# Optimization experiments

Hardware: AMD Instinct MI355X
Metric: run time of the kernel (lower is better)

The kernel has to match this reference:

```python
import jax, jax.numpy as jnp
import numpy as np

DIM = 384
HEADS = 12
HEAD_DIM = DIM // HEADS
SCALE = HEAD_DIM ** -0.5
HIDDEN = 4 * DIM
EPS = 1e-5


def _dwconv(x, w, b):
    # depthwise 3x3 conv, NCHW, kernel [C,1,3,3], groups=C
    y = jax.lax.conv_general_dilated(
        x, w, window_strides=(1, 1), padding='SAME',
        dimension_numbers=('NCHW', 'OIHW', 'NCHW'),
        feature_group_count=x.shape[1])
    return y + b[None, :, None, None]


def _layernorm(x, g, b):
    mu = jnp.mean(x, axis=-1, keepdims=True)
    var = jnp.mean(jnp.square(x - mu), axis=-1, keepdims=True)
    return (x - mu) * jax.lax.rsqrt(var + EPS) * g + b


def setup_inputs() -> dict:
    key = jax.random.key(0)
    ks = jax.random.split(key, 10)
    s = 0.02
    inp = {
        'x': jax.random.normal(ks[0], (32, DIM, 28, 28), dtype=jnp.float32),
        'cpe1_w': jax.random.normal(ks[1], (DIM, 1, 3, 3), dtype=jnp.float32) * s,
        'cpe1_b': jnp.zeros((DIM,), jnp.float32),
        'norm1_g': jnp.ones((DIM,), jnp.float32),
        'norm1_b': jnp.zeros((DIM,), jnp.float32),
        'qkv_w': jax.random.normal(ks[2], (3 * DIM, DIM), dtype=jnp.float32) * s,
        'proj_w': jax.random.normal(ks[3], (DIM, DIM), dtype=jnp.float32) * s,
        'proj_b': jnp.zeros((DIM,), jnp.float32),
        'cpe2_w': jax.random.normal(ks[4], (DIM, 1, 3, 3), dtype=jnp.float32) * s,
        'cpe2_b': jnp.zeros((DIM,), jnp.float32),
        'norm2_g': jnp.ones((DIM,), jnp.float32),
        'norm2_b': jnp.zeros((DIM,), jnp.float32),
        'fc1_w': jax.random.normal(ks[5], (HIDDEN, DIM), dtype=jnp.float32) * s,
        'fc1_b': jnp.zeros((HIDDEN,), jnp.float32),
        'fc2_w': jax.random.normal(ks[6], (DIM, HIDDEN), dtype=jnp.float32) * s,
        'fc2_b': jnp.zeros((DIM,), jnp.float32),
    }
    return inp


def reference(x, cpe1_w, cpe1_b, norm1_g, norm1_b, qkv_w, proj_w, proj_b,
              cpe2_w, cpe2_b, norm2_g, norm2_b, fc1_w, fc1_b, fc2_w, fc2_b):
    B, C, H, W = x.shape
    N = H * W
    # cpe1: depthwise conv residual (act = Identity)
    x = x + _dwconv(x, cpe1_w, cpe1_b)
    x = jnp.transpose(x.reshape(B, C, N), (0, 2, 1))  # [B, N, C]

    # channel attention
    cur = _layernorm(x, norm1_g, norm1_b)
    qkv = cur @ qkv_w.T  # [B, N, 3C]
    qkv = qkv.reshape(B, N, 3, HEADS, HEAD_DIM)
    q = qkv[:, :, 0]  # [B, N, h, d]
    k = qkv[:, :, 1] * SCALE
    v = qkv[:, :, 2]
    # attn = k^T @ v over tokens: [B, h, d, d]
    attn = jnp.einsum('bnhd,bnhe->bhde', k, v)
    attn = jax.nn.softmax(attn, axis=-1)
    # out[n,d] = sum_e attn[d,e] * q[n,e]
    out = jnp.einsum('bhde,bnhe->bnhd', attn, q).reshape(B, N, C)
    cur = out @ proj_w.T + proj_b
    x = x + cur

    # cpe2
    x = jnp.transpose(x, (0, 2, 1)).reshape(B, C, H, W)
    x = x + _dwconv(x, cpe2_w, cpe2_b)

    # MLP
    x = jnp.transpose(x.reshape(B, C, N), (0, 2, 1))  # [B, N, C]
    y = _layernorm(x, norm2_g, norm2_b)
    y = jax.nn.gelu(y @ fc1_w.T + fc1_b, approximate=False)
    y = y @ fc2_w.T + fc2_b
    x = x + y
    return jnp.transpose(x, (0, 2, 1)).reshape(B, C, H, W)
```

## Files before the change

kernel.cpp:

```cpp
#include <hip/hip_runtime.h>
#include <hip/hip_bf16.h>

#define CDIM 384
#define NHEADS 12
#define HDIM 32
#define HIDDEN 1536
#define BBATCH 32
#define HH 28
#define WW 28
#define NTOK 784
#define BN (BBATCH * NTOK)
#define LN_EPS 1e-5f
#define ATT_SCALE 0.17677669529663687f
#define YTILES 196
#define PERXCD 25

typedef __hip_bfloat16 bf16;
typedef __attribute__((ext_vector_type(8))) short bf16x8;
typedef __attribute__((ext_vector_type(4))) float f32x4;

__device__ __forceinline__ void stf(float* p, float v) { *p = v; }
__device__ __forceinline__ void stf(bf16* p, float v) { *p = __float2bfloat16(v); }

__device__ __forceinline__ short f2bs(float v) {
    bf16 t = __float2bfloat16(v);
    return *reinterpret_cast<short*>(&t);
}

__device__ __forceinline__ float bf2f(unsigned short u) {
    return __uint_as_float(((unsigned)u) << 16);
}

__device__ __forceinline__ float gelu_f(float x) {
    float u = x * (0.7978845608f + 0.0356774081f * x * x);
    float e = __expf(-2.f * u);
    return x / (1.f + e);
}

__device__ __forceinline__ void gload16(const void* g, void* l) {
    __builtin_amdgcn_global_load_lds(
        (const __attribute__((address_space(1))) unsigned int*)g,
        (__attribute__((address_space(3))) unsigned int*)l, 16, 0, 0);
}

__global__ __launch_bounds__(256) void prep_k(
    const float* __restrict__ w0, const float* __restrict__ w1,
    const float* __restrict__ w2, const float* __restrict__ w3,
    bf16* __restrict__ dst, const float* __restrict__ cw,
    float* __restrict__ cwt)
{
    int blk = blockIdx.x;
    if (blk >= 6912) {
        int i = (blk - 6912) * 256 + threadIdx.x;
        if (i < 9 * CDIM) {
            int k = i / CDIM, c = i % CDIM;
            cwt[i] = cw[c * 9 + k];
        }
        return;
    }
    int i = blk * 256 + threadIdx.x;
    const float* src; int off;
    if (i < 442368)       { src = w0; off = i; }
    else if (i < 589824)  { src = w1; off = i - 442368; }
    else if (i < 1179648) { src = w2; off = i - 589824; }
    else                  { src = w3; off = i - 1179648; }
    dst[i] = __float2bfloat16(src[off]);
}

__global__ __launch_bounds__(256) void cpe1_tr_fused(
    const float* __restrict__ x, const float* __restrict__ w,
    const float* __restrict__ bias, float* __restrict__ xt)
{
    __shared__ float sm[32][100];
    __shared__ float t[32][33];
    int b = blockIdx.z;
    int n0 = blockIdx.y * 32;
    int c0 = blockIdx.x * 32;
    int tx = threadIdx.x, ty = threadIdx.y;
    int wstart = n0 - 32;
    for (int ci = ty; ci < 32; ci += 8) {
        const float* bp = x + ((size_t)b * CDIM + c0 + ci) * NTOK;
#pragma unroll
        for (int j = 0; j < 3; j++) {
            int l = tx + j * 32;
            int n = wstart + l;
            sm[ci][l] = ((unsigned)n < NTOK) ? bp[n] : 0.f;
        }
    }
    __syncthreads();
    int n = n0 + tx;
    if (n < NTOK) {
        int h = n / WW, wc = n % WW;
        bool hm = h > 0, hp = h < HH - 1, wm = wc > 0, wpv = wc < WW - 1;
        int l = tx + 32;
        for (int ci = ty; ci < 32; ci += 8) {
            const float* wp = w + (c0 + ci) * 9;
            float s = wp[4] * sm[ci][l];
            if (hm)        s += wp[1] * sm[ci][l - WW];
            if (hp)        s += wp[7] * sm[ci][l + WW];
            if (wm)        s += wp[3] * sm[ci][l - 1];
            if (wpv)       s += wp[5] * sm[ci][l + 1];
            if (hm && wm)  s += wp[0] * sm[ci][l - WW - 1];
            if (hm && wpv) s += wp[2] * sm[ci][l - WW + 1];
            if (hp && wm)  s += wp[6] * sm[ci][l + WW - 1];
            if (hp && wpv) s += wp[8] * sm[ci][l + WW + 1];
            t[tx][ci] = sm[ci][l] + s + bias[c0 + ci];
        }
    }
    __syncthreads();
    for (int i = ty; i < 32; i += 8) {
        int nn = n0 + i;
        if (nn < NTOK)
            xt[((size_t)b * NTOK + nn) * CDIM + c0 + tx] = t[i][tx];
    }
}

__global__ __launch_bounds__(256) void ln1_k(
    const float* __restrict__ in, const float* __restrict__ g,
    const float* __restrict__ b, bf16* __restrict__ out)
{
    int tid = threadIdx.x;
    int l = tid & 31;
    size_t tok = (size_t)blockIdx.x * 8 + (tid >> 5);
    const float4* row = (const float4*)(in + tok * CDIM);
    float4 v[3];
    float s = 0.f;
#pragma unroll
    for (int j = 0; j < 3; j++) {
        v[j] = row[l + j * 32];
        s += v[j].x + v[j].y + v[j].z + v[j].w;
    }
#pragma unroll
    for (int off = 16; off >= 1; off >>= 1) s += __shfl_xor(s, off);
    float mu = s * (1.f / CDIM);
    float q = 0.f;
#pragma unroll
    for (int j = 0; j < 3; j++) {
        float dx = v[j].x - mu, dy = v[j].y - mu;
        float dz = v[j].z - mu, dw = v[j].w - mu;
        q += dx * dx + dy * dy + dz * dz + dw * dw;
    }
#pragma unroll
    for (int off = 16; off >= 1; off >>= 1) q += __shfl_xor(q, off);
    float rs = rsqrtf(q * (1.f / CDIM) + LN_EPS);
    const float4* g4 = (const float4*)g;
    const float4* b4 = (const float4*)b;
    ushort4* o4 = (ushort4*)(out + tok * CDIM);
#pragma unroll
    for (int j = 0; j < 3; j++) {
        int idx = l + j * 32;
        float4 gv = g4[idx], bv = b4[idx];
        ushort4 r;
        r.x = (unsigned short)f2bs((v[j].x - mu) * rs * gv.x + bv.x);
        r.y = (unsigned short)f2bs((v[j].y - mu) * rs * gv.y + bv.y);
        r.z = (unsigned short)f2bs((v[j].z - mu) * rs * gv.z + bv.z);
        r.w = (unsigned short)f2bs((v[j].w - mu) * rs * gv.w + bv.w);
        o4[idx] = r;
    }
}

__global__ __launch_bounds__(256) void cpe2_ln_fused(
    const float* __restrict__ xin, const float* __restrict__ wt,
    const float* __restrict__ cbias, const float* __restrict__ g,
    const float* __restrict__ b, float* __restrict__ x3,
    bf16* __restrict__ lnout)
{
    __shared__ float wts[9 * CDIM];
    int tid = threadIdx.x;
    for (int i = tid; i < 864; i += 256)
        ((float4*)wts)[i] = ((const float4*)wt)[i];
    __syncthreads();
    int l = tid & 31;
    size_t tok = (size_t)blockIdx.x * 8 + (tid >> 5);
    int n = (int)(tok % NTOK);
    int h = n / WW, wc = n % WW;
    bool hm = h > 0, hp = h < HH - 1, wm = wc > 0, wpv = wc < WW - 1;
    const float* row = xin + tok * CDIM;
    const float4* w4 = (const float4*)wts;
    float4 ctr[3], acc[3];
#pragma unroll
    for (int j = 0; j < 3; j++) {
        int idx = l + j * 32;
        ctr[j] = ((const float4*)row)[idx];
        float4 ww = w4[4 * 96 + idx];
        acc[j].x = ww.x * ctr[j].x; acc[j].y = ww.y * ctr[j].y;
        acc[j].z = ww.z * ctr[j].z; acc[j].w = ww.w * ctr[j].w;
    }
#define TAP(k, cond, dn)                                                     \
    if (cond) {                                                              \
        const float4* rp = (const float4*)(row + (dn) * CDIM);               \
        _Pragma("unroll")                                                    \
        for (int j = 0; j < 3; j++) {                                        \
            int idx = l + j * 32;                                            \
            float4 vv = rp[idx];                                             \
            float4 ww = w4[(k) * 96 + idx];                                  \
            acc[j].x = fmaf(ww.x, vv.x, acc[j].x);                           \
            acc[j].y = fmaf(ww.y, vv.y, acc[j].y);                           \
            acc[j].z = fmaf(ww.z, vv.z, acc[j].z);                           \
            acc[j].w = fmaf(ww.w, vv.w, acc[j].w);                           \
        }                                                                    \
    }
    TAP(0, hm && wm,   -WW - 1)
    TAP(1, hm,         -WW)
    TAP(2, hm && wpv,  -WW + 1)
    TAP(3, wm,         -1)
    TAP(5, wpv,        1)
    TAP(6, hp && wm,   WW - 1)
    TAP(7, hp,         WW)
    TAP(8, hp && wpv,  WW + 1)
#undef TAP
    float s = 0.f;
    float4 val[3];
    float4* x3r = (float4*)(x3 + tok * CDIM);
#pragma unroll
    for (int j = 0; j < 3; j++) {
        int idx = l + j * 32;
        float4 cb = ((const float4*)cbias)[idx];
        val[j].x = ctr[j].x + acc[j].x + cb.x;
        val[j].y = ctr[j].y + acc[j].y + cb.y;
        val[j].z = ctr[j].z + acc[j].z + cb.z;
        val[j].w = ctr[j].w + acc[j].w + cb.w;
        x3r[idx] = val[j];
        s += val[j].x + val[j].y + val[j].z + val[j].w;
    }
#pragma unroll
    for (int off = 16; off >= 1; off >>= 1) s += __shfl_xor(s, off);
    float mu = s * (1.f / CDIM);
    float q = 0.f;
#pragma unroll
    for (int j = 0; j < 3; j++) {
        float dx = val[j].x - mu, dy = val[j].y - mu;
        float dz = val[j].z - mu, dw = val[j].w - mu;
        q += dx * dx + dy * dy + dz * dz + dw * dw;
    }
#pragma unroll
    for (int off = 16; off >= 1; off >>= 1) q += __shfl_xor(q, off);
    float rs = rsqrtf(q * (1.f / CDIM) + LN_EPS);
    const float4* g4 = (const float4*)g;
    const float4* b4 = (const float4*)b;
    ushort4* o4 = (ushort4*)(lnout + tok * CDIM);
#pragma unroll
    for (int j = 0; j < 3; j++) {
        int idx = l + j * 32;
        float4 gv = g4[idx], bv = b4[idx];
        ushort4 r;
        r.x = (unsigned short)f2bs((val[j].x - mu) * rs * gv.x + bv.x);
        r.y = (unsigned short)f2bs((val[j].y - mu) * rs * gv.y + bv.y);
        r.z = (unsigned short)f2bs((val[j].z - mu) * rs * gv.z + bv.z);
        r.w = (unsigned short)f2bs((val[j].w - mu) * rs * gv.w + bv.w);
        o4[idx] = r;
    }
}

template <int ACT, bool RES, typename TO, bool OUTT, int K>
__global__ __launch_bounds__(256, 4) void gemm_mfma(
    const short* __restrict__ Abf, const short* __restrict__ Bw,
    const float* __restrict__ bias, const float* __restrict__ res,
    TO* __restrict__ Co, int M, int NX)
{
    int id = blockIdx.x;
    int xcd = id & 7, slot_ = id >> 3;
    int yloc = slot_ / NX, xx = slot_ - yloc * NX;
    int y = xcd * PERXCD + yloc;
    if (y >= YTILES) return;

    __shared__ __align__(16) short lds[16896];
    const int tid = threadIdx.x;
    const int wid = tid >> 6, lane = tid & 63;
    const int wrow = wid >> 1, wcol = wid & 1;
    const int quad = lane >> 4, lr = lane & 15;
    const int r0 = y * 128, m0 = xx * 128;

    const int srow = lane >> 2;
    const int sg   = (lane & 3) ^ ((lane >> 3) & 3);
    const short* gA = Abf + (size_t)(r0 + wid * 32 + srow) * K + sg * 8;
    const short* gB = Bw  + (size_t)(m0 + wid * 32 + srow) * K + sg * 8;

    auto stage = [&](int k0, int p) {
        short* lA = lds + p * 8192 + wid * 1024;
        short* lB = lds + p * 8192 + 4096 + wid * 1024;
#pragma unroll
        for (int k = 0; k < 2; k++) {
            gload16(gA + k0 + (size_t)k * 16 * K, lA + k * 512);
            gload16(gB + k0 + (size_t)k * 16 * K, lB + k * 512);
        }
    };

    const int slot = (quad ^ ((lr >> 1) & 3)) * 8;
    int fA[4], fB[4];
#pragma unroll
    for (int i = 0; i < 4; i++) {
        fA[i] = (wrow * 64 + i * 16 + lr) * 32 + slot;
        fB[i] = 4096 + (wcol * 64 + i * 16 + lr) * 32 + slot;
    }

    f32x4 acc[4][4] = {};

    stage(0, 0);
    int p = 0;
    for (int k0 = 0; k0 < K; k0 += 32) {
        __syncthreads();
        if (k0 + 32 < K) stage(k0 + 32, p ^ 1);
        const short* As = lds + p * 8192;
        bf16x8 av[4], bv[4];
#pragma unroll
        for (int i = 0; i < 4; i++) {
            av[i] = *(const bf16x8*)(As + fA[i]);
            bv[i] = *(const bf16x8*)(As + fB[i]);
        }
#pragma unroll
        for (int i = 0; i < 4; i++)
#pragma unroll
            for (int j = 0; j < 4; j++)
                acc[i][j] = __builtin_amdgcn_mfma_f32_16x16x32_bf16(
                    av[i], bv[j], acc[i][j], 0, 0, 0);
        p ^= 1;
    }

    if constexpr (OUTT) {
        float* Csf = (float*)lds;
        __syncthreads();
#pragma unroll
        for (int pass = 0; pass < 2; pass++) {
            if (wcol == pass) {
#pragma unroll
                for (int i = 0; i < 4; i++) {
                    int lrow = wrow * 64 + i * 16 + quad * 4;
#pragma unroll
                    for (int j = 0; j < 4; j++) {
                        int lcol = j * 16 + lr;
                        int gc = m0 + pass * 64 + lcol;
                        float bb = bias ? bias[gc] : 0.f;
#pragma unroll
                        for (int rr = 0; rr < 4; rr++) {
                            float v = acc[i][j][rr] + bb;
                            if (RES)
                                v += res[(size_t)(r0 + lrow + rr) * M + gc];
                            if (ACT == 1) v = gelu_f(v);
                            Csf[(lrow + rr) * 66 + lcol] = v;
                        }
                    }
                }
            }
            __syncthreads();
            int tok = tid & 127;
            int csel = tid >> 7;
            int gtok = r0 + tok;
            int bb2 = gtok / NTOK;
            int nn2 = gtok - bb2 * NTOK;
#pragma unroll
            for (int s = 0; s < 32; s++) {
                int cl = s * 2 + csel;
                int gcol = m0 + pass * 64 + cl;
                Co[((size_t)bb2 * CDIM + gcol) * NTOK + nn2] = Csf[tok * 66 + cl];
            }
            __syncthreads();
        }
    } else if constexpr (sizeof(TO) == 4) {
#pragma unroll
        for (int i = 0; i < 4; i++) {
            int gr = r0 + wrow * 64 + i * 16 + quad * 4;
#pragma unroll
            for (int j = 0; j < 4; j++) {
                int gc = m0 + wcol * 64 + j * 16 + lr;
                float bb = bias ? bias[gc] : 0.f;
#pragma unroll
                for (int rr = 0; rr < 4; rr++) {
                    size_t idx = (size_t)(gr + rr) * M + gc;
                    float v = acc[i][j][rr] + bb;
                    if (RES) v += res[idx];
                    if (ACT == 1) v = gelu_f(v);
                    stf((float*)&Co[idx], v);
                }
            }
        }
    } else {
        __syncthreads();
        short* Cs = lds;
#pragma unroll
        for (int i = 0; i < 4; i++) {
            int lrow = wrow * 64 + i * 16 + quad * 4;
#pragma unroll
            for (int j = 0; j < 4; j++) {
                int lcol = wcol * 64 + j * 16 + lr;
                float bb = bias ? bias[m0 + lcol] : 0.f;
#pragma unroll
                for (int rr = 0; rr < 4; rr++) {
                    float v = acc[i][j][rr] + bb;
                    if (ACT == 1) v = gelu_f(v);
                    Cs[(lrow + rr) * 132 + lcol] = f2bs(v);
                }
            }
        }
        __syncthreads();
        short* co = (short*)Co;
#pragma unroll
        for (int s = 0; s < 16; s++) {
            int row = s * 8 + (tid >> 5);
            int seg = tid & 31;
            uint2 vv = *(const uint2*)(Cs + row * 132 + seg * 4);
            *(uint2*)(co + (size_t)(r0 + row) * M + m0 + seg * 4) = vv;
        }
    }
}

__global__ __launch_bounds__(256) void attn_k(
    const bf16* __restrict__ qkv, float* __restrict__ attn)
{
    int bh = blockIdx.x;
    int b = bh / NHEADS, h = bh % NHEADS;
    __shared__ float ks[64][32];
    __shared__ float vs[64][32];
    __shared__ float sm[32][33];
    int tid = threadIdx.x;
    int d = tid >> 3, e0 = (tid & 7) * 4;
    int nn = tid >> 2, q8 = (tid & 3) * 8;
    float acc[4] = {0.f, 0.f, 0.f, 0.f};
    for (int n0 = 0; n0 < NTOK; n0 += 64) {
        int n = n0 + nn;
        float kv[8], vv[8];
        if (n < NTOK) {
            const unsigned short* base =
                (const unsigned short*)qkv + ((size_t)b * NTOK + n) * (3 * CDIM);
            uint4 kq = *(const uint4*)(base + CDIM + h * HDIM + q8);
            uint4 vq = *(const uint4*)(base + 2 * CDIM + h * HDIM + q8);
            const unsigned short* kp = (const unsigned short*)&kq;
            const unsigned short* vp = (const unsigned short*)&vq;
#pragma unroll
            for (int j = 0; j < 8; j++) {
                kv[j] = ATT_SCALE * bf2f(kp[j]);
                vv[j] = bf2f(vp[j]);
            }
        } else {
#pragma unroll
            for (int j = 0; j < 8; j++) { kv[j] = 0.f; vv[j] = 0.f; }
        }
        *(float4*)&ks[nn][q8]     = make_float4(kv[0], kv[1], kv[2], kv[3]);
        *(float4*)&ks[nn][q8 + 4] = make_float4(kv[4], kv[5], kv[6], kv[7]);
        *(float4*)&vs[nn][q8]     = make_float4(vv[0], vv[1], vv[2], vv[3]);
        *(float4*)&vs[nn][q8 + 4] = make_float4(vv[4], vv[5], vv[6], vv[7]);
        __syncthreads();
#pragma unroll 8
        for (int k = 0; k < 64; k++) {
            float kd = ks[k][d];
            float4 vv4 = *(const float4*)&vs[k][e0];
            acc[0] = fmaf(kd, vv4.x, acc[0]);
            acc[1] = fmaf(kd, vv4.y, acc[1]);
            acc[2] = fmaf(kd, vv4.z, acc[2]);
            acc[3] = fmaf(kd, vv4.w, acc[3]);
        }
        __syncthreads();
    }
#pragma unroll
    for (int j = 0; j < 4; j++) sm[d][e0 + j] = acc[j];
    __syncthreads();
    if (tid < 32) {
        float mx = -1e30f;
#pragma unroll
        for (int e = 0; e < 32; e++) mx = fmaxf(mx, sm[tid][e]);
        float ssum = 0.f;
        float ex[32];
#pragma unroll
        for (int e = 0; e < 32; e++) { ex[e] = expf(sm[tid][e] - mx); ssum += ex[e]; }
        float inv = 1.f / ssum;
        float* arow = attn + ((size_t)bh * 32 + tid) * 32;
#pragma unroll
        for (int e = 0; e < 32; e++) arow[e] = ex[e] * inv;
    }
}

__global__ __launch_bounds__(384) void apply_attn_k(
    const bf16* __restrict__ qkv, const float* __restrict__ attn,
    bf16* __restrict__ out)
{
    int b = blockIdx.x;
    int chunk = blockIdx.y;
    int tid = threadIdx.x;
    int h = tid >> 5;
    __shared__ float qs[8][CDIM];
    float at[32];
    const float4* ap = (const float4*)(attn + ((size_t)(b * NHEADS) * 32 + tid) * 32);
#pragma unroll
    for (int e4 = 0; e4 < 8; e4++) {
        float4 v = ap[e4];
        at[e4 * 4 + 0] = v.x; at[e4 * 4 + 1] = v.y;
        at[e4 * 4 + 2] = v.z; at[e4 * 4 + 3] = v.w;
    }
    int row8 = tid / 48;
    int seg = tid - row8 * 48;
    int nbase = chunk * 56;
    for (int t0 = 0; t0 < 56; t0 += 8) {
        __syncthreads();
        {
            int n = nbase + t0 + row8;
            const unsigned short* src =
                (const unsigned short*)qkv + ((size_t)b * NTOK + n) * (3 * CDIM) + seg * 8;
            uint4 qv = *(const uint4*)src;
            const unsigned short* qp = (const unsigned short*)&qv;
            *(float4*)&qs[row8][seg * 8] =
                make_float4(bf2f(qp[0]), bf2f(qp[1]), bf2f(qp[2]), bf2f(qp[3]));
            *(float4*)&qs[row8][seg * 8 + 4] =
                make_float4(bf2f(qp[4]), bf2f(qp[5]), bf2f(qp[6]), bf2f(qp[7]));
        }
        __syncthreads();
#pragma unroll
        for (int i = 0; i < 8; i++) {
            const float4* q4 = (const float4*)&qs[i][h * 32];
            float s = 0.f;
#pragma unroll
            for (int e4 = 0; e4 < 8; e4++) {
                float4 qv = q4[e4];
                s = fmaf(at[e4 * 4 + 0], qv.x, s);
                s = fmaf(at[e4 * 4 + 1], qv.y, s);
                s = fmaf(at[e4 * 4 + 2], qv.z, s);
                s = fmaf(at[e4 * 4 + 3], qv.w, s);
            }
            int n = nbase + t0 + i;
            out[((size_t)b * NTOK + n) * CDIM + tid] = __float2bfloat16(s);
        }
    }
}

extern "C" void kernel_launch(void* const* d_in, const int* in_sizes, int n_in,
                              void* d_out, int out_size, void* d_ws, size_t ws_size,
                              hipStream_t stream) {
    const float* x      = (const float*)d_in[0];
    const float* cpe1_w = (const float*)d_in[1];
    const float* cpe1_b = (const float*)d_in[2];
    const float* n1g    = (const float*)d_in[3];
    const float* n1b    = (const float*)d_in[4];
    const float* qkv_w  = (const float*)d_in[5];
    const float* proj_w = (const float*)d_in[6];
    const float* proj_b = (const float*)d_in[7];
    const float* cpe2_w = (const float*)d_in[8];
    const float* cpe2_b = (const float*)d_in[9];
    const float* n2g    = (const float*)d_in[10];
    const float* n2b    = (const float*)d_in[11];
    const float* fc1_w  = (const float*)d_in[12];
    const float* fc1_b  = (const float*)d_in[13];
    const float* fc2_w  = (const float*)d_in[14];
    const float* fc2_b  = (const float*)d_in[15];

    const size_t A = (size_t)BN * CDIM;
    const size_t HA = A / 2;

    bf16* wqkv  = (bf16*)d_ws;
    bf16* wproj = wqkv + 442368;
    bf16* wfc1  = wproj + 147456;
    bf16* wfc2  = wfc1 + 589824;
    float* base = (float*)d_ws + 884736;

    float* xt        = base;
    bf16*  curb      = (bf16*)(base + A);
    bf16*  ylnb      = (bf16*)(base + A);
    bf16*  qkvb      = (bf16*)(base + A + HA);
    float* x3        = base + A + HA;
    bf16*  h1        = (bf16*)(base + A + HA + A);
    float* attnm     = base + 3 * A;
    bf16*  attn_outb = (bf16*)(base + 3 * A + 393216);
    float* cpe2_wt   = base + (A * 9) / 2;

    const int GEMM_GRID3  = 8 * PERXCD * 3;
    const int GEMM_GRID9  = 8 * PERXCD * 9;
    const int GEMM_GRID12 = 8 * PERXCD * 12;

    prep_k<<<6926, 256, 0, stream>>>(qkv_w, proj_w, fc1_w, fc2_w, wqkv,
                                     cpe2_w, cpe2_wt);

    cpe1_tr_fused<<<dim3(CDIM / 32, 25, BBATCH), dim3(32, 8), 0, stream>>>(
        x, cpe1_w, cpe1_b, xt);
    ln1_k<<<BN / 8, 256, 0, stream>>>(xt, n1g, n1b, curb);
    gemm_mfma<0, false, bf16, false, 384><<<GEMM_GRID9, 256, 0, stream>>>(
        (const short*)curb, (const short*)wqkv, nullptr, nullptr, qkvb, 1152, 9);
    attn_k<<<BBATCH * NHEADS, 256, 0, stream>>>(qkvb, attnm);
    apply_attn_k<<<dim3(BBATCH, 14), 384, 0, stream>>>(qkvb, attnm, attn_outb);
    gemm_mfma<0, true, float, false, 384><<<GEMM_GRID3, 256, 0, stream>>>(
        (const short*)attn_outb, (const short*)wproj, proj_b, xt, xt, 384, 3);
    cpe2_ln_fused<<<BN / 8, 256, 0, stream>>>(xt, cpe2_wt, cpe2_b, n2g, n2b,
                                              x3, ylnb);
    gemm_mfma<1, false, bf16, false, 384><<<GEMM_GRID12, 256, 0, stream>>>(
        (const short*)ylnb, (const short*)wfc1, fc1_b, nullptr, h1, 1536, 12);
    gemm_mfma<0, true, float, true, 1536><<<GEMM_GRID3, 256, 0, stream>>>(
        (const short*)h1, (const short*)wfc2, fc2_b, x3, (float*)d_out, 384, 3);
}
```

Baseline: 434.2 us.

## Widen cpe1 transpose tiles with float4 I/O and halve GEMM epilogue LDS

```diff
diff --git a/kernel.cpp b/kernel.cpp
--- a/kernel.cpp
+++ b/kernel.cpp
@@ -67,51 +67,65 @@
     dst[i] = __float2bfloat16(src[off]);
 }
 
-__global__ __launch_bounds__(256) void cpe1_tr_fused(
+__global__ __launch_bounds__(256) void cpe1_tr_v2(
     const float* __restrict__ x, const float* __restrict__ w,
     const float* __restrict__ bias, float* __restrict__ xt)
 {
-    __shared__ float sm[32][100];
-    __shared__ float t[32][33];
+    __shared__ float sm[64][128];
+    __shared__ float t2[64][69];
     int b = blockIdx.z;
-    int n0 = blockIdx.y * 32;
-    int c0 = blockIdx.x * 32;
-    int tx = threadIdx.x, ty = threadIdx.y;
-    int wstart = n0 - 32;
-    for (int ci = ty; ci < 32; ci += 8) {
-        const float* bp = x + ((size_t)b * CDIM + c0 + ci) * NTOK;
-#pragma unroll
-        for (int j = 0; j < 3; j++) {
-            int l = tx + j * 32;
-            int n = wstart + l;
-            sm[ci][l] = ((unsigned)n < NTOK) ? bp[n] : 0.f;
-        }
+    int n0 = blockIdx.y * 64;
+    int c0 = blockIdx.x * 64;
+    int tid = threadIdx.x;
+    int nf0 = (n0 - 32) >> 2;
+
+    const float4* xb = (const float4*)(x + ((size_t)b * CDIM + c0) * NTOK);
+#pragma unroll
+    for (int i = 0; i < 8; i++) {
+        int q = tid + i * 256;
+        int row = q >> 5, c4 = q & 31;
+        int nf = nf0 + c4;
+        float4 v = {0.f, 0.f, 0.f, 0.f};
+        if ((unsigned)nf < (NTOK / 4)) v = xb[row * (NTOK / 4) + nf];
+        *(float4*)&sm[row][c4 * 4] = v;
     }
     __syncthreads();
-    int n = n0 + tx;
+
+    int n_loc = tid & 63;
+    int n = n0 + n_loc;
+    int l = 32 + n_loc;
     if (n < NTOK) {
         int h = n / WW, wc = n % WW;
         bool hm = h > 0, hp = h < HH - 1, wm = wc > 0, wpv = wc < WW - 1;
-        int l = tx + 32;
-        for (int ci = ty; ci < 32; ci += 8) {
-            const float* wp = w + (c0 + ci) * 9;
-            float s = wp[4] * sm[ci][l];
-            if (hm)        s += wp[1] * sm[ci][l - WW];
-            if (hp)        s += wp[7] * sm[ci][l + WW];
-            if (wm)        s += wp[3] * sm[ci][l - 1];
-            if (wpv)       s += wp[5] * sm[ci][l + 1];
-            if (hm && wm)  s += wp[0] * sm[ci][l - WW - 1];
-            if (hm && wpv) s += wp[2] * sm[ci][l - WW + 1];
-            if (hp && wm)  s += wp[6] * sm[ci][l + WW - 1];
-            if (hp && wpv) s += wp[8] * sm[ci][l + WW + 1];
-            t[tx][ci] = sm[ci][l] + s + bias[c0 + ci];
+        int cbase = tid >> 6;
+#pragma unroll
+        for (int j = 0; j < 16; j++) {
+            int c_loc = cbase + j * 4;
+            const float* wp = w + (c0 + c_loc) * 9;
+            const float* s = sm[c_loc];
+            float a = wp[4] * s[l];
+            if (hm)        a += wp[1] * s[l - WW];
+            if (hp)        a += wp[7] * s[l + WW];
+            if (wm)        a += wp[3] * s[l - 1];
+            if (wpv)       a += wp[5] * s[l + 1];
+            if (hm && wm)  a += wp[0] * s[l - WW - 1];
+            if (hm && wpv) a += wp[2] * s[l - WW + 1];
+            if (hp && wm)  a += wp[6] * s[l + WW - 1];
+            if (hp && wpv) a += wp[8] * s[l + WW + 1];
+            t2[n_loc][c_loc] = s[l] + a + bias[c0 + c_loc];
         }
     }
     __syncthreads();
-    for (int i = ty; i < 32; i += 8) {
-        int nn = n0 + i;
-        if (nn < NTOK)
-            xt[((size_t)b * NTOK + nn) * CDIM + c0 + tx] = t[i][tx];
+
+#pragma unroll
+    for (int i = 0; i < 4; i++) {
+        int q = tid + i * 256;
+        int nl = q >> 4, c4 = q & 15;
+        int nn = n0 + nl;
+        if (nn < NTOK) {
+            float4 v = *(const float4*)&t2[nl][c4 * 4];
+            *(float4*)(xt + ((size_t)b * NTOK + nn) * CDIM + c0 + c4 * 4) = v;
+        }
     }
 }
 
@@ -264,7 +278,7 @@
     int y = xcd * PERXCD + yloc;
     if (y >= YTILES) return;
 
-    __shared__ __align__(16) short lds[16896];
+    __shared__ __align__(16) short lds[OUTT ? 16896 : 16384];
     const int tid = threadIdx.x;
     const int wid = tid >> 6, lane = tid & 63;
     const int wrow = wid >> 1, wcol = wid & 1;
@@ -377,29 +391,35 @@
     } else {
         __syncthreads();
         short* Cs = lds;
-#pragma unroll
-        for (int i = 0; i < 4; i++) {
-            int lrow = wrow * 64 + i * 16 + quad * 4;
-#pragma unroll
-            for (int j = 0; j < 4; j++) {
-                int lcol = wcol * 64 + j * 16 + lr;
-                float bb = bias ? bias[m0 + lcol] : 0.f;
-#pragma unroll
-                for (int rr = 0; rr < 4; rr++) {
-                    float v = acc[i][j][rr] + bb;
-                    if (ACT == 1) v = gelu_f(v);
-                    Cs[(lrow + rr) * 132 + lcol] = f2bs(v);
+        short* co = (short*)Co;
+#pragma unroll
+        for (int pass = 0; pass < 2; pass++) {
+            if (wrow == pass) {
+#pragma unroll
+                for (int i = 0; i < 4; i++) {
+                    int lrow = i * 16 + quad * 4;
+#pragma unroll
+                    for (int j = 0; j < 4; j++) {
+                        int lcol = wcol * 64 + j * 16 + lr;
+                        float bb = bias ? bias[m0 + lcol] : 0.f;
+#pragma unroll
+                        for (int rr = 0; rr < 4; rr++) {
+                            float v = acc[i][j][rr] + bb;
+                            if (ACT == 1) v = gelu_f(v);
+                            Cs[(lrow + rr) * 132 + lcol] = f2bs(v);
+                        }
+                    }
                 }
             }
-        }
-        __syncthreads();
-        short* co = (short*)Co;
-#pragma unroll
-        for (int s = 0; s < 16; s++) {
-            int row = s * 8 + (tid >> 5);
-            int seg = tid & 31;
-            uint2 vv = *(const uint2*)(Cs + row * 132 + seg * 4);
-            *(uint2*)(co + (size_t)(r0 + row) * M + m0 + seg * 4) = vv;
+            __syncthreads();
+#pragma unroll
+            for (int s = 0; s < 8; s++) {
+                int row = s * 8 + (tid >> 5);
+                int seg = tid & 31;
+                uint2 vv = *(const uint2*)(Cs + row * 132 + seg * 4);
+                *(uint2*)(co + (size_t)(r0 + pass * 64 + row) * M + m0 + seg * 4) = vv;
+            }
+            __syncthreads();
         }
     }
 }
@@ -567,7 +587,7 @@
     prep_k<<<6926, 256, 0, stream>>>(qkv_w, proj_w, fc1_w, fc2_w, wqkv,
                                      cpe2_w, cpe2_wt);
 
-    cpe1_tr_fused<<<dim3(CDIM / 32, 25, BBATCH), dim3(32, 8), 0, stream>>>(
+    cpe1_tr_v2<<<dim3(CDIM / 64, 13, BBATCH), 256, 0, stream>>>(
         x, cpe1_w, cpe1_b, xt);
     ln1_k<<<BN / 8, 256, 0, stream>>>(xt, n1g, n1b, curb);
     gemm_mfma<0, false, bf16, false, 384><<<GEMM_GRID9, 256, 0, stream>>>(
```

After: 450.9 us. 3.8% more time.
